# Kernel optimization log

Hardware: AMD Instinct MI355X
Metric: run time of the kernel (lower is better)

## Reference

```python
import jax, jax.numpy as jnp
from jax import lax
import numpy as np


def _cum_masks(nd):
    # 4 nested cumulative masks over a 9-tap kernel: borders p=3,2,1,0
    ms = []
    for p in (3, 2, 1, 0):
        m = np.zeros((9,) * nd, np.float32)
        sl = tuple(slice(p, 9 - p) for _ in range(nd))
        m[sl] = 1.0
        ms.append(m)
    return jnp.asarray(np.stack(ms))  # (4, 9) or (4, 9, 9)


def _group_norm(x, w, b, groups, eps=1e-5):
    B, C, H, W = x.shape
    xg = x.reshape(B, groups, C // groups, H, W)
    mu = jnp.mean(xg, axis=(2, 3, 4), keepdims=True)
    var = jnp.var(xg, axis=(2, 3, 4), keepdims=True)
    xg = (xg - mu) * lax.rsqrt(var + eps)
    return xg.reshape(B, C, H, W) * w[None, :, None, None] + b[None, :, None, None]


def setup_inputs() -> dict:
    key = jax.random.key(0)
    ks = jax.random.split(key, 16)
    C = 256
    c = C // 4
    x = jax.random.normal(ks[0], (16, C, 128, 128), jnp.float32)
    W1 = jax.random.normal(ks[1], (1, 1, 9, 1, 1), jnp.float32)
    W2 = jax.random.normal(ks[2], (c, 1, 9, 9), jnp.float32)
    conv1_w = jax.random.normal(ks[3], (c, C, 1, 1), jnp.float32) * 0.05
    conv1_b = jax.random.normal(ks[4], (c,), jnp.float32) * 0.05
    conv2_w = jax.random.normal(ks[5], (C, c, 1, 1), jnp.float32) * 0.05
    conv2_b = jax.random.normal(ks[6], (C,), jnp.float32) * 0.05
    gn1_w = jnp.ones((c,), jnp.float32)
    gn1_b = jnp.zeros((c,), jnp.float32)
    gns_w = jnp.ones((c,), jnp.float32)
    gns_b = jnp.zeros((c,), jnp.float32)
    gn2_w = jnp.ones((C,), jnp.float32)
    gn2_b = jnp.zeros((C,), jnp.float32)
    return dict(x=x, W1=W1, W2=W2, conv1_w=conv1_w, conv1_b=conv1_b,
                conv2_w=conv2_w, conv2_b=conv2_b, gn1_w=gn1_w, gn1_b=gn1_b,
                gns_w=gns_w, gns_b=gns_b, gn2_w=gn2_w, gn2_b=gn2_b)


def reference(x, W1, W2, conv1_w, conv1_b, conv2_w, conv2_b,
              gn1_w, gn1_b, gns_w, gns_b, gn2_w, gn2_b):
    res = x
    # 1x1 conv + GN (bottleneck)
    h1 = jnp.einsum('bchw,oc->bohw', x, conv1_w[:, :, 0, 0]) + conv1_b[None, :, None, None]
    h1 = _group_norm(h1, gn1_w, gn1_b, 16)
    c = h1.shape[1]

    # --- branch A: multi-ring 1D conv along channel dim (conv3d, kernel (9,1,1)) ---
    m1 = _cum_masks(1)                                   # (4,9) cumulative masks
    r1 = m1 - jnp.concatenate([jnp.zeros_like(m1[:1]), m1[:-1]], 0)  # rings
    k1 = W1[0, 0, :, 0, 0]                               # (9,)
    a1 = jax.nn.softmax(jnp.sum(k1[None, :] * r1, 1) / (jnp.sum(r1, 1) + 1e-10))
    # linearity: softmax-weighted sum of 4 masked convs == one conv with weighted mask
    W1_eff = W1 * jnp.sum(a1[:, None] * m1, 0)[None, None, :, None, None]
    x3 = lax.conv_general_dilated(
        h1[:, None], W1_eff, (1, 1, 1), [(4, 4), (0, 0), (0, 0)],
        dimension_numbers=('NCDHW', 'OIDHW', 'NCDHW'))[:, 0]  # (b,c,h,w)

    # --- branch B: multi-ring 9x9 depthwise conv2d ---
    m2 = _cum_masks(2)                                   # (4,9,9)
    r2 = m2 - jnp.concatenate([jnp.zeros_like(m2[:1]), m2[:-1]], 0)
    num2 = jnp.sum(W2[None] * r2[:, None, None], axis=(1, 2, 3, 4))
    den2 = c * jnp.sum(r2, axis=(1, 2)) + 1e-10          # mask is (c,1,9,9) in torch
    a2 = jax.nn.softmax(num2 / den2)
    W2_eff = W2 * jnp.sum(a2[:, None, None] * m2, 0)[None, None]
    x_sa = lax.conv_general_dilated(
        h1, W2_eff, (1, 1), [(4, 4), (4, 4)],
        dimension_numbers=('NCHW', 'OIHW', 'NCHW'), feature_group_count=c)

    h = jax.nn.relu(_group_norm(x3 + x_sa, gns_w, gns_b, 16))
    out = jnp.einsum('bchw,oc->bohw', h, conv2_w[:, :, 0, 0]) + conv2_b[None, :, None, None]
    out = jax.nn.relu(_group_norm(out, gn2_w, gn2_b, 16))
    return out + res
```

## Files before the change

### kernel.cpp

```cpp
#include <hip/hip_runtime.h>
#include <math.h>

#define HW   16384
#define CC   256
#define cC   64
#define BB   16
#define CHW  (CC*HW)
#define cHW  (cC*HW)

#define WS_TB    0
#define WS_H1B   8388608
#define WS_RAWB  16777216
#define WS_W2E   50331648
#define WS_K1E   (WS_W2E + 5184)
#define WS_GN1A  (WS_K1E + 16)
#define WS_GNSA  (WS_GN1A + 512)
#define WS_GN2A  (WS_GNSA + 512)
#define WS_W1P   (WS_GN2A + 512)
#define WS_W2P   (WS_W1P + 8192)

typedef __attribute__((ext_vector_type(8))) short bf16x8;
typedef __attribute__((ext_vector_type(4))) float f32x4;

__device__ inline unsigned short f2bf(float f) {
    union { float f; unsigned u; } c; c.f = f;
    unsigned r = c.u + 0x7FFFu + ((c.u >> 16) & 1u);
    return (unsigned short)(r >> 16);
}
__device__ inline float bf2f(unsigned short h) {
    union { unsigned u; float f; } c; c.u = ((unsigned)h) << 16; return c.f;
}

__global__ void k_setup(const float* __restrict__ W1, const float* __restrict__ W2,
                        const float* __restrict__ c1w, const float* __restrict__ c2w,
                        float* __restrict__ k1e, float* __restrict__ w2e,
                        float* __restrict__ accz, unsigned short* __restrict__ w1p,
                        unsigned short* __restrict__ w2p) {
    __shared__ float tapsum[81];
    __shared__ float a2s[4];
    int tdx = threadIdx.x;
    for (int i = tdx; i < 1536; i += 128) accz[i] = 0.f;
    for (int e = tdx; e < 16384; e += 128) {
        int fi = e >> 9, rem = e & 511;
        int l = rem >> 3, j = rem & 7;
        int ks = fi >> 2, nf = fi & 3;
        int c = ks * 32 + (l >> 4) * 8 + j;
        int oc = nf * 16 + (l & 15);
        w1p[e] = f2bf(c1w[oc * 256 + c]);
    }
    for (int e = tdx; e < 16384; e += 128) {
        int fi = e >> 9, rem = e & 511;
        int l = rem >> 3, j = rem & 7;
        int ks = fi >> 4, nfg = fi & 15;
        int c = ks * 32 + (l >> 4) * 8 + j;
        int oc = nfg * 16 + (l & 15);
        w2p[e] = f2bf(c2w[oc * 64 + c]);
    }
    if (tdx < 81) {
        float s = 0.f;
        for (int ch = 0; ch < 64; ++ch) s += W2[ch * 81 + tdx];
        tapsum[tdx] = s;
    }
    __syncthreads();
    if (tdx == 0) {
        float ring[4] = {0.f, 0.f, 0.f, 0.f};
        for (int i = 0; i < 9; ++i)
            for (int j = 0; j < 9; ++j) {
                int d = max(abs(i - 4), abs(j - 4));
                int r = (d <= 1) ? 0 : (d - 1);
                ring[r] += tapsum[i * 9 + j];
            }
        float den2[4] = {576.f, 1024.f, 1536.f, 2048.f};
        float v[4], mx = -1e30f;
        for (int p = 0; p < 4; ++p) { v[p] = ring[p] / den2[p]; mx = fmaxf(mx, v[p]); }
        float se = 0.f;
        for (int p = 0; p < 4; ++p) { v[p] = expf(v[p] - mx); se += v[p]; }
        for (int p = 0; p < 4; ++p) a2s[p] = v[p] / se;
        float k1[9];
        for (int k = 0; k < 9; ++k) k1[k] = W1[k];
        float num[4];
        num[0] = k1[3] + k1[4] + k1[5];
        num[1] = k1[2] + k1[6];
        num[2] = k1[1] + k1[7];
        num[3] = k1[0] + k1[8];
        float den1[4] = {3.f, 2.f, 2.f, 2.f};
        mx = -1e30f;
        for (int p = 0; p < 4; ++p) { v[p] = num[p] / den1[p]; mx = fmaxf(mx, v[p]); }
        se = 0.f;
        for (int p = 0; p < 4; ++p) { v[p] = expf(v[p] - mx); se += v[p]; }
        float a1[4];
        for (int p = 0; p < 4; ++p) a1[p] = v[p] / se;
        float s1arr[5];
        s1arr[0] = 1.f; s1arr[1] = 1.f;
        s1arr[4] = a1[3]; s1arr[3] = a1[2] + a1[3]; s1arr[2] = a1[1] + s1arr[3];
        for (int k = 0; k < 9; ++k) { int d = abs(k - 4); k1e[k] = k1[k] * s1arr[d]; }
    }
    __syncthreads();
    float s2arr[5];
    s2arr[0] = 1.f; s2arr[1] = 1.f;
    s2arr[4] = a2s[3]; s2arr[3] = a2s[2] + a2s[3]; s2arr[2] = a2s[1] + s2arr[3];
    for (int idx = tdx; idx < 64 * 81; idx += 128) {
        int tap = idx % 81;
        int i = tap / 9, j = tap - i * 9;
        int d = max(abs(i - 4), abs(j - 4));
        w2e[idx] = W2[idx] * s2arr[d];
    }
}

__device__ inline void gn_affine(const float* __restrict__ acc, int b, int g,
                                 float inv_n, const float* __restrict__ gw,
                                 const float* __restrict__ gb, int ch,
                                 float& sc, float& sh) {
    float s = acc[(b * 16 + g) * 2], ss = acc[(b * 16 + g) * 2 + 1];
    float mu = s * inv_n;
    float var = ss * inv_n - mu * mu;
    float rstd = rsqrtf(var + 1e-5f);
    sc = gw[ch] * rstd;
    sh = gb[ch] - mu * sc;
}

__global__ __launch_bounds__(256) void k_conv1(const float* __restrict__ x,
        const unsigned short* __restrict__ w1p, const float* __restrict__ b1,
        unsigned short* __restrict__ h1, float* __restrict__ gn1a) {
    int bid = blockIdx.x;
    int b = bid >> 6, pt = bid & 63;
    int tid = threadIdx.x;
    int w = tid >> 6, lane = tid & 63;
    int l15 = lane & 15, lg = lane >> 4;
    int p_wave = pt * 256 + w * 64;
    const bf16x8* w1v = (const bf16x8*)w1p;
    f32x4 acc[4][4];
#pragma unroll
    for (int mf = 0; mf < 4; ++mf)
#pragma unroll
        for (int nf = 0; nf < 4; ++nf) acc[mf][nf] = (f32x4){0.f, 0.f, 0.f, 0.f};
    const float* xb = x + b * CHW;
#pragma unroll 1
    for (int ks = 0; ks < 8; ++ks) {
        int c0 = ks * 32 + lg * 8;
        bf16x8 afr[4];
#pragma unroll
        for (int mf = 0; mf < 4; ++mf) {
            const float* xp = xb + c0 * HW + p_wave + mf * 16 + l15;
            bf16x8 a;
#pragma unroll
            for (int j = 0; j < 8; ++j) a[j] = (short)f2bf(__builtin_nontemporal_load(xp + j * HW));
            afr[mf] = a;
        }
#pragma unroll
        for (int nf = 0; nf < 4; ++nf) {
            bf16x8 bfr = w1v[(ks * 4 + nf) * 64 + lane];
#pragma unroll
            for (int mf = 0; mf < 4; ++mf)
                acc[mf][nf] = __builtin_amdgcn_mfma_f32_16x16x32_bf16(afr[mf], bfr, acc[mf][nf], 0, 0, 0);
        }
    }
    __shared__ float red[4][16][2];
    unsigned short* hb = h1 + b * cHW;
#pragma unroll
    for (int nf = 0; nf < 4; ++nf) {
        int oc = nf * 16 + l15;
        float bias = b1[oc];
        float s = 0.f, ss = 0.f;
#pragma unroll
        for (int mf = 0; mf < 4; ++mf) {
            f32x4 v = acc[mf][nf];
            v[0] += bias; v[1] += bias; v[2] += bias; v[3] += bias;
            ushort4 hv = make_ushort4(f2bf(v[0]), f2bf(v[1]), f2bf(v[2]), f2bf(v[3]));
            *(ushort4*)(hb + oc * HW + p_wave + mf * 16 + lg * 4) = hv;
            s += v[0] + v[1] + v[2] + v[3];
            ss += v[0] * v[0] + v[1] * v[1] + v[2] * v[2] + v[3] * v[3];
        }
        s += __shfl_xor(s, 16, 64); ss += __shfl_xor(ss, 16, 64);
        s += __shfl_xor(s, 32, 64); ss += __shfl_xor(ss, 32, 64);
        s += __shfl_xor(s, 1, 64);  ss += __shfl_xor(ss, 1, 64);
        s += __shfl_xor(s, 2, 64);  ss += __shfl_xor(ss, 2, 64);
        if (lg == 0 && (l15 & 3) == 0) {
            int g = nf * 4 + (l15 >> 2);
            red[w][g][0] = s; red[w][g][1] = ss;
        }
    }
    __syncthreads();
    if (tid < 32) {
        int g = tid >> 1, c = tid & 1;
        float v = red[0][g][c] + red[1][g][c] + red[2][g][c] + red[3][g][c];
        atomicAdd(&gn1a[(b * 16 + g) * 2 + c], v);
    }
}

__global__ __launch_bounds__(256) void k_x3(const unsigned short* __restrict__ h1,
        const float* __restrict__ gn1a, const float* __restrict__ g1w,
        const float* __restrict__ g1b, const float* __restrict__ k1e,
        unsigned short* __restrict__ t) {
    int i = blockIdx.x * 256 + threadIdx.x;
    int b = i >> 13, p = (i & 8191) * 2;
    __shared__ float lsc[64], lsh[64], lke[9];
    if (threadIdx.x < 64) {
        int ch = threadIdx.x;
        float sc, sh;
        gn_affine(gn1a, b, ch >> 2, 1.f / 65536.f, g1w, g1b, ch, sc, sh);
        lsc[ch] = sc; lsh[ch] = sh;
    }
    if (threadIdx.x < 9) lke[threadIdx.x] = k1e[threadIdx.x];
    __syncthreads();
    const unsigned short* hb = h1 + b * cHW + p;
    float2 win[9];
#pragma unroll
    for (int k = 0; k < 9; ++k) {
        int ch = k - 4;
        if (ch >= 0) {
            ushort2 hv = *(const ushort2*)(hb + ch * HW);
            float s = lsc[ch], h = lsh[ch];
            win[k] = make_float2(fmaf(bf2f(hv.x), s, h), fmaf(bf2f(hv.y), s, h));
        } else win[k] = make_float2(0.f, 0.f);
    }
    unsigned short* tb = t + b * cHW + p;
#pragma unroll
    for (int ch = 0; ch < 64; ++ch) {
        float2 s = make_float2(0.f, 0.f);
#pragma unroll
        for (int k = 0; k < 9; ++k) {
            float kv = lke[k];
            s.x = fmaf(win[k].x, kv, s.x);
            s.y = fmaf(win[k].y, kv, s.y);
        }
        *(ushort2*)(tb + ch * HW) = make_ushort2(f2bf(s.x), f2bf(s.y));
#pragma unroll
        for (int k = 0; k < 8; ++k) win[k] = win[k + 1];
        int nc = ch + 5;
        if (nc < 64) {
            ushort2 hv = *(const ushort2*)(hb + nc * HW);
            float sN = lsc[nc], hN = lsh[nc];
            win[8] = make_float2(fmaf(bf2f(hv.x), sN, hN), fmaf(bf2f(hv.y), sN, hN));
        } else win[8] = make_float2(0.f, 0.f);
    }
}

__global__ __launch_bounds__(256) void k_xsa(const unsigned short* __restrict__ h1,
        const float* __restrict__ gn1a, const float* __restrict__ g1w,
        const float* __restrict__ g1b, const float* __restrict__ w2e,
        unsigned short* __restrict__ t, float* __restrict__ gnsa) {
    int bid = blockIdx.x;
    int b = bid >> 8, ch = (bid >> 2) & 63, rt = bid & 3;
    int r0 = rt * 32;
    int tid = threadIdx.x;
    float sc, sh;
    gn_affine(gn1a, b, ch >> 2, 1.f / 65536.f, g1w, g1b, ch, sc, sh);
    const unsigned short* hp = h1 + b * cHW + ch * HW;
    __shared__ float tile[40 * 136];
    for (int li = tid; li < 40 * 34; li += 256) {
        int row = li / 34, c4 = li - row * 34;
        int col = c4 * 4;
        int gr = r0 - 4 + row;
        float4 z = make_float4(0.f, 0.f, 0.f, 0.f);
        if (gr >= 0 && gr < 128 && c4 >= 1 && c4 <= 32) {
            int gc = col - 4;
            ushort4 hv = *(const ushort4*)(hp + gr * 128 + gc);
            z = make_float4(fmaf(bf2f(hv.x), sc, sh), fmaf(bf2f(hv.y), sc, sh),
                            fmaf(bf2f(hv.z), sc, sh), fmaf(bf2f(hv.w), sc, sh));
        }
        *(float4*)&tile[row * 136 + col] = z;
    }
    __syncthreads();
    int r4g = tid >> 5, c4g = tid & 31;
    int orow0 = r4g * 4, oc0 = c4g * 4;
    const float* wch = w2e + ch * 81;
    float acc[4][4];
#pragma unroll
    for (int r = 0; r < 4; ++r)
#pragma unroll
        for (int k = 0; k < 4; ++k) acc[r][k] = 0.f;
#pragma unroll
    for (int d = 0; d < 12; ++d) {
        const float* lr = &tile[(orow0 + d) * 136 + oc0];
        float v[12];
        *(float4*)&v[0] = *(const float4*)lr;
        *(float4*)&v[4] = *(const float4*)(lr + 4);
        *(float4*)&v[8] = *(const float4*)(lr + 8);
#pragma unroll
        for (int r = 0; r < 4; ++r) {
            if (r <= d && d - r <= 8) {
                const int i = d - r;
#pragma unroll
                for (int j = 0; j < 9; ++j) {
                    float wv = wch[i * 9 + j];
                    acc[r][0] = fmaf(v[j + 0], wv, acc[r][0]);
                    acc[r][1] = fmaf(v[j + 1], wv, acc[r][1]);
                    acc[r][2] = fmaf(v[j + 2], wv, acc[r][2]);
                    acc[r][3] = fmaf(v[j + 3], wv, acc[r][3]);
                }
            }
        }
    }
    float s = 0.f, ss = 0.f;
    unsigned short* tpb = t + b * cHW + ch * HW + (r0 + orow0) * 128 + oc0;
#pragma unroll
    for (int r = 0; r < 4; ++r) {
        unsigned short* tp = tpb + r * 128;
        ushort4 tv = *(const ushort4*)tp;
        float r0v = bf2f(tv.x) + acc[r][0];
        float r1v = bf2f(tv.y) + acc[r][1];
        float r2v = bf2f(tv.z) + acc[r][2];
        float r3v = bf2f(tv.w) + acc[r][3];
        *(ushort4*)tp = make_ushort4(f2bf(r0v), f2bf(r1v), f2bf(r2v), f2bf(r3v));
        s += r0v + r1v + r2v + r3v;
        ss += r0v * r0v + r1v * r1v + r2v * r2v + r3v * r3v;
    }
#pragma unroll
    for (int off = 32; off; off >>= 1) { s += __shfl_xor(s, off, 64); ss += __shfl_xor(ss, off, 64); }
    __shared__ float rs[4], rss[4];
    int lane = tid & 63, wv2 = tid >> 6;
    if (lane == 0) { rs[wv2] = s; rss[wv2] = ss; }
    __syncthreads();
    if (tid == 0) {
        int gi = (b * 16 + (ch >> 2)) * 2;
        atomicAdd(&gnsa[gi], rs[0] + rs[1] + rs[2] + rs[3]);
        atomicAdd(&gnsa[gi + 1], rss[0] + rss[1] + rss[2] + rss[3]);
    }
}

__global__ __launch_bounds__(256) void k_conv2(const unsigned short* __restrict__ t,
        const float* __restrict__ gnsa, const float* __restrict__ gsw,
        const float* __restrict__ gsb, const unsigned short* __restrict__ w2p,
        const float* __restrict__ b2, unsigned short* __restrict__ raw,
        float* __restrict__ gn2a) {
    int bid = blockIdx.x;
    int obk = bid & 1, pt = (bid >> 1) & 127, b = bid >> 8;
    int tid = threadIdx.x;
    int w = tid >> 6, lane = tid & 63;
    int l15 = lane & 15, lg = lane >> 4;
    int pw = w >> 1, ow = w & 1;
    int p_wave = pt * 128 + pw * 64;
    __shared__ float lsc[64], lsh[64];
    __shared__ float red[4][4][2];
    if (tid < 64) {
        float sc, sh;
        gn_affine(gnsa, b, tid >> 2, 1.f / 65536.f, gsw, gsb, tid, sc, sh);
        lsc[tid] = sc; lsh[tid] = sh;
    }
    __syncthreads();
    const bf16x8* w2v = (const bf16x8*)w2p;
    f32x4 acc[4][4];
#pragma unroll
    for (int mf = 0; mf < 4; ++mf)
#pragma unroll
        for (int nf = 0; nf < 4; ++nf) acc[mf][nf] = (f32x4){0.f, 0.f, 0.f, 0.f};
    const unsigned short* tb = t + b * cHW;
#pragma unroll
    for (int ks = 0; ks < 2; ++ks) {
        int kb = ks * 32 + lg * 8;
        float kc[8], kh[8];
#pragma unroll
        for (int j = 0; j < 8; ++j) { kc[j] = lsc[kb + j]; kh[j] = lsh[kb + j]; }
        bf16x8 afr[4];
#pragma unroll
        for (int mf = 0; mf < 4; ++mf) {
            const unsigned short* tp = tb + kb * HW + p_wave + mf * 16 + l15;
            bf16x8 a;
#pragma unroll
            for (int j = 0; j < 8; ++j) {
                float v = fmaxf(fmaf(bf2f(tp[j * HW]), kc[j], kh[j]), 0.f);
                a[j] = (short)f2bf(v);
            }
            afr[mf] = a;
        }
#pragma unroll
        for (int nf = 0; nf < 4; ++nf) {
            int fi = ks * 16 + (obk * 8 + ow * 4 + nf);
            bf16x8 bfr = w2v[fi * 64 + lane];
#pragma unroll
            for (int mf = 0; mf < 4; ++mf)
                acc[mf][nf] = __builtin_amdgcn_mfma_f32_16x16x32_bf16(afr[mf], bfr, acc[mf][nf], 0, 0, 0);
        }
    }
    int oc0 = obk * 128 + ow * 64;
    unsigned short* ob = raw + b * CHW;
    float sred[4], ssred[4];
#pragma unroll
    for (int nf = 0; nf < 4; ++nf) {
        int oc = oc0 + nf * 16 + l15;
        float bias = b2[oc];
        float s = 0.f, ss = 0.f;
#pragma unroll
        for (int mf = 0; mf < 4; ++mf) {
            f32x4 v = acc[mf][nf];
            v[0] += bias; v[1] += bias; v[2] += bias; v[3] += bias;
            ushort4 hv = make_ushort4(f2bf(v[0]), f2bf(v[1]), f2bf(v[2]), f2bf(v[3]));
            *(ushort4*)(ob + oc * HW + p_wave + mf * 16 + lg * 4) = hv;
            s += v[0] + v[1] + v[2] + v[3];
            ss += v[0] * v[0] + v[1] * v[1] + v[2] * v[2] + v[3] * v[3];
        }
#pragma unroll
        for (int off = 32; off; off >>= 1) { s += __shfl_xor(s, off, 64); ss += __shfl_xor(ss, off, 64); }
        sred[nf] = s; ssred[nf] = ss;
    }
    if (lane == 0) {
#pragma unroll
        for (int nf = 0; nf < 4; ++nf) { red[w][nf][0] = sred[nf]; red[w][nf][1] = ssred[nf]; }
    }
    __syncthreads();
    if (tid < 16) {
        int ow2 = tid >> 3, nf = (tid >> 1) & 3, c = tid & 1;
        float v = red[ow2][nf][c] + red[ow2 + 2][nf][c];
        int g = obk * 8 + ow2 * 4 + nf;
        atomicAdd(&gn2a[(b * 16 + g) * 2 + c], v);
    }
}

__global__ __launch_bounds__(256) void k_final(const float* __restrict__ x,
        const unsigned short* __restrict__ raw, const float* __restrict__ gn2a,
        const float* __restrict__ g2w, const float* __restrict__ g2b,
        float* __restrict__ out) {
    int tid = blockIdx.x * blockDim.x + threadIdx.x;
    const int total4 = (BB * CHW) / 4;
    int stride = gridDim.x * blockDim.x;
    for (int i = tid; i < total4; i += stride) {
        int e = i * 4;
        int b = e >> 22;
        int o = (e >> 14) & 255;
        float s, h;
        gn_affine(gn2a, b, o >> 4, 1.f / 262144.f, g2w, g2b, o, s, h);
        ushort4 rv = ((const ushort4*)raw)[i];
        f32x4 xv = __builtin_nontemporal_load((const f32x4*)x + i);
        f32x4 r;
        r[0] = fmaxf(fmaf(bf2f(rv.x), s, h), 0.f) + xv[0];
        r[1] = fmaxf(fmaf(bf2f(rv.y), s, h), 0.f) + xv[1];
        r[2] = fmaxf(fmaf(bf2f(rv.z), s, h), 0.f) + xv[2];
        r[3] = fmaxf(fmaf(bf2f(rv.w), s, h), 0.f) + xv[3];
        __builtin_nontemporal_store(r, (f32x4*)out + i);
    }
}

extern "C" void kernel_launch(void* const* d_in, const int* in_sizes, int n_in,
                              void* d_out, int out_size, void* d_ws, size_t ws_size,
                              hipStream_t stream) {
    (void)in_sizes; (void)n_in; (void)out_size; (void)ws_size;
    const float* x   = (const float*)d_in[0];
    const float* W1  = (const float*)d_in[1];
    const float* W2  = (const float*)d_in[2];
    const float* c1w = (const float*)d_in[3];
    const float* c1b = (const float*)d_in[4];
    const float* c2w = (const float*)d_in[5];
    const float* c2b = (const float*)d_in[6];
    const float* g1w = (const float*)d_in[7];
    const float* g1b = (const float*)d_in[8];
    const float* gsw = (const float*)d_in[9];
    const float* gsb = (const float*)d_in[10];
    const float* g2w = (const float*)d_in[11];
    const float* g2b = (const float*)d_in[12];
    float* out = (float*)d_out;
    float* ws  = (float*)d_ws;

    unsigned short* tb   = (unsigned short*)(ws + WS_TB);
    unsigned short* h1b  = (unsigned short*)(ws + WS_H1B);
    unsigned short* rawb = (unsigned short*)(ws + WS_RAWB);
    float* w2e  = ws + WS_W2E;
    float* k1e  = ws + WS_K1E;
    float* gn1a = ws + WS_GN1A;
    float* gnsa = ws + WS_GNSA;
    float* gn2a = ws + WS_GN2A;
    unsigned short* w1p = (unsigned short*)(ws + WS_W1P);
    unsigned short* w2p = (unsigned short*)(ws + WS_W2P);

    k_setup<<<1, 128, 0, stream>>>(W1, W2, c1w, c2w, k1e, w2e, gn1a, w1p, w2p);
    k_conv1<<<1024, 256, 0, stream>>>(x, w1p, c1b, h1b, gn1a);
    k_x3<<<512, 256, 0, stream>>>(h1b, gn1a, g1w, g1b, k1e, tb);
    k_xsa<<<4096, 256, 0, stream>>>(h1b, gn1a, g1w, g1b, w2e, tb, gnsa);
    k_conv2<<<4096, 256, 0, stream>>>(tb, gnsa, gsw, gsb, w2p, c2b, rawb, gn2a);
    k_final<<<4096, 256, 0, stream>>>(x, rawb, gn2a, g2w, g2b, out);
}
```

Measured before the change: 344.7 us.

## Stage normalized activations in LDS once per block and retile conv2 output channels

k_conv2 now gives each block a 64-pixel tile and all 256 output channels, with the four waves splitting the output channels. Each block loads its 64x64 activation tile from global memory once, applies the GroupNorm affine and ReLU there, and writes it to padded shared memory. Every wave then reads its MFMA operands from shared memory. Before, the strided global gathers and the normalize math were repeated across the two output-channel halves and the two wave columns. The cost is an extra barrier and about 8.7KB of LDS per block, with some risk of LDS bank conflicts on the strided 2-byte reads.

```diff
diff --git a/kernel.cpp b/kernel.cpp
--- a/kernel.cpp
+++ b/kernel.cpp
@@ -319,19 +319,21 @@
     }
 }
 
+#define ROWU 68
+
 __global__ __launch_bounds__(256) void k_conv2(const unsigned short* __restrict__ t,
         const float* __restrict__ gnsa, const float* __restrict__ gsw,
         const float* __restrict__ gsb, const unsigned short* __restrict__ w2p,
         const float* __restrict__ b2, unsigned short* __restrict__ raw,
         float* __restrict__ gn2a) {
     int bid = blockIdx.x;
-    int obk = bid & 1, pt = (bid >> 1) & 127, b = bid >> 8;
+    int b = bid >> 8, pt = bid & 255;
+    int p0 = pt * 64;
     int tid = threadIdx.x;
     int w = tid >> 6, lane = tid & 63;
     int l15 = lane & 15, lg = lane >> 4;
-    int pw = w >> 1, ow = w & 1;
-    int p_wave = pt * 128 + pw * 64;
     __shared__ float lsc[64], lsh[64];
+    __shared__ unsigned short tps[64 * ROWU];
     __shared__ float red[4][4][2];
     if (tid < 64) {
         float sc, sh;
@@ -339,41 +341,57 @@
         lsc[tid] = sc; lsh[tid] = sh;
     }
     __syncthreads();
+    {
+        int ch = tid >> 2, c8 = tid & 3;
+        float sc = lsc[ch], sh = lsh[ch];
+        const unsigned short* tg = t + b * cHW + ch * HW + p0;
+#pragma unroll
+        for (int half = 0; half < 2; ++half) {
+            int off = (c8 + half * 4) * 8;
+            ushort4 a0 = *(const ushort4*)(tg + off);
+            ushort4 a1 = *(const ushort4*)(tg + off + 4);
+            ushort4 o0, o1;
+            o0.x = f2bf(fmaxf(fmaf(bf2f(a0.x), sc, sh), 0.f));
+            o0.y = f2bf(fmaxf(fmaf(bf2f(a0.y), sc, sh), 0.f));
+            o0.z = f2bf(fmaxf(fmaf(bf2f(a0.z), sc, sh), 0.f));
+            o0.w = f2bf(fmaxf(fmaf(bf2f(a0.w), sc, sh), 0.f));
+            o1.x = f2bf(fmaxf(fmaf(bf2f(a1.x), sc, sh), 0.f));
+            o1.y = f2bf(fmaxf(fmaf(bf2f(a1.y), sc, sh), 0.f));
+            o1.z = f2bf(fmaxf(fmaf(bf2f(a1.z), sc, sh), 0.f));
+            o1.w = f2bf(fmaxf(fmaf(bf2f(a1.w), sc, sh), 0.f));
+            *(ushort4*)(&tps[ch * ROWU + off]) = o0;
+            *(ushort4*)(&tps[ch * ROWU + off + 4]) = o1;
+        }
+    }
+    __syncthreads();
     const bf16x8* w2v = (const bf16x8*)w2p;
     f32x4 acc[4][4];
 #pragma unroll
     for (int mf = 0; mf < 4; ++mf)
 #pragma unroll
         for (int nf = 0; nf < 4; ++nf) acc[mf][nf] = (f32x4){0.f, 0.f, 0.f, 0.f};
-    const unsigned short* tb = t + b * cHW;
 #pragma unroll
     for (int ks = 0; ks < 2; ++ks) {
         int kb = ks * 32 + lg * 8;
-        float kc[8], kh[8];
-#pragma unroll
-        for (int j = 0; j < 8; ++j) { kc[j] = lsc[kb + j]; kh[j] = lsh[kb + j]; }
         bf16x8 afr[4];
 #pragma unroll
         for (int mf = 0; mf < 4; ++mf) {
-            const unsigned short* tp = tb + kb * HW + p_wave + mf * 16 + l15;
+            int pos = mf * 16 + l15;
             bf16x8 a;
 #pragma unroll
-            for (int j = 0; j < 8; ++j) {
-                float v = fmaxf(fmaf(bf2f(tp[j * HW]), kc[j], kh[j]), 0.f);
-                a[j] = (short)f2bf(v);
-            }
+            for (int j = 0; j < 8; ++j) a[j] = (short)tps[(kb + j) * ROWU + pos];
             afr[mf] = a;
         }
 #pragma unroll
         for (int nf = 0; nf < 4; ++nf) {
-            int fi = ks * 16 + (obk * 8 + ow * 4 + nf);
+            int fi = ks * 16 + (w * 4 + nf);
             bf16x8 bfr = w2v[fi * 64 + lane];
 #pragma unroll
             for (int mf = 0; mf < 4; ++mf)
                 acc[mf][nf] = __builtin_amdgcn_mfma_f32_16x16x32_bf16(afr[mf], bfr, acc[mf][nf], 0, 0, 0);
         }
     }
-    int oc0 = obk * 128 + ow * 64;
+    int oc0 = w * 64;
     unsigned short* ob = raw + b * CHW;
     float sred[4], ssred[4];
 #pragma unroll
@@ -386,7 +404,7 @@
             f32x4 v = acc[mf][nf];
             v[0] += bias; v[1] += bias; v[2] += bias; v[3] += bias;
             ushort4 hv = make_ushort4(f2bf(v[0]), f2bf(v[1]), f2bf(v[2]), f2bf(v[3]));
-            *(ushort4*)(ob + oc * HW + p_wave + mf * 16 + lg * 4) = hv;
+            *(ushort4*)(ob + oc * HW + p0 + mf * 16 + lg * 4) = hv;
             s += v[0] + v[1] + v[2] + v[3];
             ss += v[0] * v[0] + v[1] * v[1] + v[2] * v[2] + v[3] * v[3];
         }
@@ -399,11 +417,10 @@
         for (int nf = 0; nf < 4; ++nf) { red[w][nf][0] = sred[nf]; red[w][nf][1] = ssred[nf]; }
     }
     __syncthreads();
-    if (tid < 16) {
-        int ow2 = tid >> 3, nf = (tid >> 1) & 3, c = tid & 1;
-        float v = red[ow2][nf][c] + red[ow2 + 2][nf][c];
-        int g = obk * 8 + ow2 * 4 + nf;
-        atomicAdd(&gn2a[(b * 16 + g) * 2 + c], v);
+    if (tid < 32) {
+        int w_ = tid >> 3, nf = (tid >> 1) & 3, c = tid & 1;
+        int g = w_ * 4 + nf;
+        atomicAdd(&gn2a[(b * 16 + g) * 2 + c], red[w_][nf][c]);
     }
 }
 
```

Result: no change. 342.2 us (-0.7%).
